# Kernel optimization log

Hardware: AMD Instinct MI355X
Metric: run time of the kernel (lower is better)

## Reference

```python
import jax, jax.numpy as jnp
import numpy as np

NORM = 20.0   # from dataset 'NETS'
ALPHA = 1.0
EPS = 1e-12   # torch F.normalize eps


def _l2_normalize(x):
    n = jnp.sqrt(jnp.sum(x * x, axis=-1, keepdims=True))
    return x / jnp.maximum(n, EPS)


def setup_inputs() -> dict:
    key = jax.random.key(0)
    k1, k2, k3, k4, k5 = jax.random.split(key, 5)
    B, P, C = 4096, 32, 512
    predicted_score = jax.random.uniform(k1, (B,), dtype=jnp.float32) * NORM
    targets = jax.random.uniform(k2, (B,), dtype=jnp.float32) * NORM
    feats = jax.random.normal(k3, (B, C), dtype=jnp.float32)
    pivot_features = jax.random.normal(k4, (B, P, C), dtype=jnp.float32)
    pivot_scores = jax.random.uniform(k5, (B, P), dtype=jnp.float32) * NORM
    return {
        "predicted_score": predicted_score,
        "targets": targets,
        "feats": feats,
        "pivot_features": pivot_features,
        "pivot_scores": pivot_scores,
    }


def reference(predicted_score, targets, feats, pivot_features, pivot_scores):
    scale = ALPHA * NORM
    f = _l2_normalize(feats)                      # (B, C)
    pf = _l2_normalize(pivot_features)            # (B, P, C)
    ps = pivot_scores.astype(jnp.float32)         # (B, P)

    # image-text: (B,1,C) @ (B,C,P) -> (B,P)
    it_matches = jnp.einsum('bc,bpc->bp', f, pf)
    it_label = 1.0 - 2.0 * jnp.abs(targets[:, None] - ps) / scale
    image_text_loss = jnp.mean(jnp.abs(it_matches - it_label))

    # image-image: (B,B)
    ii_matches = f @ f.T
    ii_label = 1.0 - 2.0 * jnp.abs(targets[:, None] - targets[None, :]) / scale
    image_image_loss = jnp.mean(jnp.abs(ii_matches - ii_label))

    # text-text: (B,P,P)
    tt_matches = jnp.einsum('bpc,bqc->bpq', pf, pf)
    tt_label = 1.0 - 2.0 * jnp.abs(ps[:, :, None] - ps[:, None, :]) / scale
    text_text_loss = jnp.mean(jnp.abs(tt_matches - tt_label))

    mae_loss = jnp.mean(jnp.abs(predicted_score - targets))

    return (image_image_loss, text_text_loss, image_text_loss, mae_loss)
```

## Files before the change

kernel.cpp:

```cpp
#include <hip/hip_runtime.h>
#include <hip/hip_bf16.h>
#include <stdint.h>

#define B_N 4096
#define P_N 32
#define C_N 512
#define LABC 0.1f

typedef float  floatx4 __attribute__((ext_vector_type(4)));
typedef __bf16 bf16x8  __attribute__((ext_vector_type(8)));

__device__ __forceinline__ unsigned short f2bf(float x) {
    return __builtin_bit_cast(unsigned short, __float2bfloat16(x));
}
__device__ __forceinline__ float bf2f(unsigned short b) {
    return __builtin_bit_cast(float, ((unsigned int)b) << 16);
}

__device__ __forceinline__ void bfly_reduce2(float& a, float& b) {
#pragma unroll
    for (int m = 1; m < 64; m <<= 1) {
        a += __shfl_xor(a, m, 64);
        b += __shfl_xor(b, m, 64);
    }
}
__device__ __forceinline__ void bfly_reduce1(float& a) {
#pragma unroll
    for (int m = 1; m < 64; m <<= 1) a += __shfl_xor(a, m, 64);
}

__global__ void k_init(double* acc) {
    if (threadIdx.x < 3) acc[threadIdx.x] = 0.0;
}

__global__ __launch_bounds__(256) void k_norm_feats(const float* __restrict__ feats,
                                                    unsigned short* __restrict__ fb) {
    const int wave = threadIdx.x >> 6, lane = threadIdx.x & 63;
    const int row = blockIdx.x * 4 + wave;
    const float* src = feats + (size_t)row * C_N + lane * 8;
    float4 v0 = *(const float4*)src;
    float4 v1 = *(const float4*)(src + 4);
    float ss = v0.x*v0.x + v0.y*v0.y + v0.z*v0.z + v0.w*v0.w
             + v1.x*v1.x + v1.y*v1.y + v1.z*v1.z + v1.w*v1.w;
    bfly_reduce1(ss);
    const float inv = rsqrtf(fmaxf(ss, 1e-24f));
    unsigned short o[8];
    o[0] = f2bf(v0.x*inv); o[1] = f2bf(v0.y*inv); o[2] = f2bf(v0.z*inv); o[3] = f2bf(v0.w*inv);
    o[4] = f2bf(v1.x*inv); o[5] = f2bf(v1.y*inv); o[6] = f2bf(v1.z*inv); o[7] = f2bf(v1.w*inv);
    uint4 pk;
    pk.x = (unsigned)o[0] | ((unsigned)o[1] << 16);
    pk.y = (unsigned)o[2] | ((unsigned)o[3] << 16);
    pk.z = (unsigned)o[4] | ((unsigned)o[5] << 16);
    pk.w = (unsigned)o[6] | ((unsigned)o[7] << 16);
    *(uint4*)(fb + (size_t)row * C_N + lane * 8) = pk;
}

#define CH_STRIDE 33
__global__ __launch_bounds__(256) void k_tt_it(const float* __restrict__ pf_g,
                                               const float* __restrict__ ps_g,
                                               const float* __restrict__ targets,
                                               const unsigned short* __restrict__ fb,
                                               double* __restrict__ acc) {
    __shared__ __align__(16) unsigned short pfs[64 * CH_STRIDE * 8];
    __shared__ float psS[P_N];
    __shared__ float redT[4], redI[4];

    const int b = blockIdx.x;
    const int tid = threadIdx.x, wave = tid >> 6, lane = tid & 63;
    const int quad = lane >> 4, l15 = lane & 15;

    if (tid < P_N) psS[tid] = ps_g[b * P_N + tid];
    const float tb = targets[b];

    uint4 fraw = *(const uint4*)(fb + (size_t)b * C_N + lane * 8);
    const unsigned short* fbits = (const unsigned short*)&fraw;
    float fr[8];
#pragma unroll
    for (int j = 0; j < 8; ++j) fr[j] = bf2f(fbits[j]);

    float it_sum = 0.f;
    const float* base = pf_g + (size_t)b * P_N * C_N;

#pragma unroll
    for (int i = 0; i < 8; ++i) {
        const int r = wave * 8 + i;
        const float* src = base + r * C_N + lane * 8;
        float4 v0 = *(const float4*)src;
        float4 v1 = *(const float4*)(src + 4);
        float pv[8] = {v0.x, v0.y, v0.z, v0.w, v1.x, v1.y, v1.z, v1.w};
        float ss = 0.f, fd = 0.f;
#pragma unroll
        for (int j = 0; j < 8; ++j) { ss += pv[j]*pv[j]; fd += pv[j]*fr[j]; }
        bfly_reduce2(ss, fd);
        const float inv = rsqrtf(fmaxf(ss, 1e-24f));
        unsigned short o[8];
#pragma unroll
        for (int j = 0; j < 8; ++j) o[j] = f2bf(pv[j] * inv);
        uint4 pk;
        pk.x = (unsigned)o[0] | ((unsigned)o[1] << 16);
        pk.y = (unsigned)o[2] | ((unsigned)o[3] << 16);
        pk.z = (unsigned)o[4] | ((unsigned)o[5] << 16);
        pk.w = (unsigned)o[6] | ((unsigned)o[7] << 16);
        *(uint4*)&pfs[((size_t)lane * CH_STRIDE + r) * 8] = pk;
        if (lane == 0) {
            const float lab = 1.f - LABC * fabsf(tb - ps_g[b * P_N + r]);
            it_sum += fabsf(fd * inv - lab);
        }
    }
    __syncthreads();

    const int pt = (wave >> 1) * 16, qt = (wave & 1) * 16;
    floatx4 acc4 = {0.f, 0.f, 0.f, 0.f};
#pragma unroll
    for (int kk = 0; kk < 16; ++kk) {
        const int ch = kk * 4 + quad;
        bf16x8 a = __builtin_bit_cast(bf16x8, *(const uint4*)&pfs[((size_t)ch * CH_STRIDE + pt + l15) * 8]);
        bf16x8 bb = __builtin_bit_cast(bf16x8, *(const uint4*)&pfs[((size_t)ch * CH_STRIDE + qt + l15) * 8]);
        acc4 = __builtin_amdgcn_mfma_f32_16x16x32_bf16(a, bb, acc4, 0, 0, 0);
    }
    float tt_sum = 0.f;
#pragma unroll
    for (int r = 0; r < 4; ++r) {
        const int p = pt + quad * 4 + r;
        const int q = qt + l15;
        const float lab = 1.f - LABC * fabsf(psS[p] - psS[q]);
        tt_sum += fabsf(acc4[r] - lab);
    }

    bfly_reduce2(tt_sum, it_sum);
    if (lane == 0) { redT[wave] = tt_sum; redI[wave] = it_sum; }
    __syncthreads();
    if (tid == 0) {
        atomicAdd(&acc[1], (double)(redT[0] + redT[1] + redT[2] + redT[3]));
        atomicAdd(&acc[2], (double)(redI[0] + redI[1] + redI[2] + redI[3]));
    }
}

#define APAD 130
__global__ __launch_bounds__(256) void k_ii(const unsigned short* __restrict__ fb,
                                            const float* __restrict__ targets,
                                            double* __restrict__ acc) {
    const int bm = blockIdx.y, bn = blockIdx.x;
    if (bn < bm) return;
    __shared__ __align__(16) unsigned short As[4 * APAD * 8];
    __shared__ __align__(16) unsigned short Bs[4 * APAD * 8];
    __shared__ float tmS[128], tnS[128];
    __shared__ float red[4];

    const int tid = threadIdx.x, wave = tid >> 6, lane = tid & 63;
    const int quad = lane >> 4, l15 = lane & 15;
    const int wr = wave >> 1, wc = wave & 1;
    const int mbase = bm * 128, nbase = bn * 128;

    if (tid < 128) tmS[tid] = targets[mbase + tid];
    else           tnS[tid - 128] = targets[nbase + tid - 128];

    const int row = tid >> 1, half = tid & 1;
    const unsigned short* aSrc = fb + (size_t)(mbase + row) * C_N + half * 16;
    const unsigned short* bSrc = fb + (size_t)(nbase + row) * C_N + half * 16;
    const int c0 = half * 2, c1 = half * 2 + 1;

    floatx4 accv[16];
#pragma unroll
    for (int i = 0; i < 16; ++i) accv[i] = (floatx4){0.f, 0.f, 0.f, 0.f};

    uint4 a0 = *(const uint4*)(aSrc);
    uint4 a1 = *(const uint4*)(aSrc + 8);
    uint4 b0 = *(const uint4*)(bSrc);
    uint4 b1 = *(const uint4*)(bSrc + 8);

    for (int ks = 0; ks < 16; ++ks) {
        __syncthreads();
        *(uint4*)&As[((size_t)c0 * APAD + row) * 8] = a0;
        *(uint4*)&As[((size_t)c1 * APAD + row) * 8] = a1;
        *(uint4*)&Bs[((size_t)c0 * APAD + row) * 8] = b0;
        *(uint4*)&Bs[((size_t)c1 * APAD + row) * 8] = b1;
        __syncthreads();
        if (ks < 15) {
            const int off = (ks + 1) * 32;
            a0 = *(const uint4*)(aSrc + off);
            a1 = *(const uint4*)(aSrc + off + 8);
            b0 = *(const uint4*)(bSrc + off);
            b1 = *(const uint4*)(bSrc + off + 8);
        }
        bf16x8 af[4], bfv[4];
#pragma unroll
        for (int t = 0; t < 4; ++t)
            af[t] = __builtin_bit_cast(bf16x8, *(const uint4*)&As[((size_t)quad * APAD + wr * 64 + t * 16 + l15) * 8]);
#pragma unroll
        for (int t = 0; t < 4; ++t)
            bfv[t] = __builtin_bit_cast(bf16x8, *(const uint4*)&Bs[((size_t)quad * APAD + wc * 64 + t * 16 + l15) * 8]);
#pragma unroll
        for (int ti = 0; ti < 4; ++ti)
#pragma unroll
            for (int tj = 0; tj < 4; ++tj)
                accv[ti * 4 + tj] = __builtin_amdgcn_mfma_f32_16x16x32_bf16(af[ti], bfv[tj], accv[ti * 4 + tj], 0, 0, 0);
    }

    float s = 0.f;
#pragma unroll
    for (int ti = 0; ti < 4; ++ti) {
#pragma unroll
        for (int tj = 0; tj < 4; ++tj) {
#pragma unroll
            for (int r = 0; r < 4; ++r) {
                const int p = wr * 64 + ti * 16 + quad * 4 + r;
                const int q = wc * 64 + tj * 16 + l15;
                const float lab = 1.f - LABC * fabsf(tmS[p] - tnS[q]);
                s += fabsf(accv[ti * 4 + tj][r] - lab);
            }
        }
    }
    if (bm != bn) s *= 2.f;
    bfly_reduce1(s);
    if (lane == 0) red[wave] = s;
    __syncthreads();
    if (tid == 0) atomicAdd(&acc[0], (double)(red[0] + red[1] + red[2] + red[3]));
}

__global__ __launch_bounds__(256) void k_final(const float* __restrict__ pred,
                                               const float* __restrict__ targ,
                                               const double* __restrict__ acc,
                                               float* __restrict__ out) {
    __shared__ float red[4];
    const int tid = threadIdx.x, wave = tid >> 6, lane = tid & 63;
    float s = 0.f;
    for (int i = tid; i < B_N; i += 256) s += fabsf(pred[i] - targ[i]);
    bfly_reduce1(s);
    if (lane == 0) red[wave] = s;
    __syncthreads();
    if (tid == 0) {
        const float mae = (red[0] + red[1] + red[2] + red[3]) * (1.f / B_N);
        out[0] = (float)(acc[0] / (double)((size_t)B_N * B_N));
        out[1] = (float)(acc[1] / (double)((size_t)B_N * P_N * P_N));
        out[2] = (float)(acc[2] / (double)((size_t)B_N * P_N));
        out[3] = mae;
    }
}

extern "C" void kernel_launch(void* const* d_in, const int* in_sizes, int n_in,
                              void* d_out, int out_size, void* d_ws, size_t ws_size,
                              hipStream_t stream) {
    const float* pred  = (const float*)d_in[0];
    const float* targ  = (const float*)d_in[1];
    const float* feats = (const float*)d_in[2];
    const float* pf    = (const float*)d_in[3];
    const float* ps    = (const float*)d_in[4];
    float* out = (float*)d_out;

    double* acc = (double*)d_ws;
    unsigned short* fb = (unsigned short*)((char*)d_ws + 256);

    k_init<<<1, 64, 0, stream>>>(acc);
    k_norm_feats<<<B_N / 4, 256, 0, stream>>>(feats, fb);
    k_tt_it<<<B_N, 256, 0, stream>>>(pf, ps, targ, fb, acc);
    k_ii<<<dim3(32, 32), 256, 0, stream>>>(fb, targ, acc);
    k_final<<<1, 256, 0, stream>>>(pred, targ, acc, out);
}
```

Baseline: 448.6 us.

## Fuse ii and tt/it kernels into one launch, normalize pivots via Gram diagonal

Merges the image-image GEMM blocks (upper triangle only, 528 blocks) and the per-sample text-text/image-text blocks into a single kernel sharing a union of shared memory. Pivot features are packed to bf16 unnormalized, and norms come from the Gram matrix diagonal. The image-text dot products are computed with an extra MFMA instead of butterfly reductions. Init and MAE partial sums fold into the prep kernel, cutting launches from five to three and removing per-row shuffle reductions. The risk is extra bf16 rounding because pivots are normalized after the bf16 matmul.

```diff
diff --git a/kernel.cpp b/kernel.cpp
--- a/kernel.cpp
+++ b/kernel.cpp
@@ -6,6 +6,7 @@
 #define P_N 32
 #define C_N 512
 #define LABC 0.1f
+#define N_II 528
 
 typedef float  floatx4 __attribute__((ext_vector_type(4)));
 typedef __bf16 bf16x8  __attribute__((ext_vector_type(8)));
@@ -13,10 +14,14 @@
 __device__ __forceinline__ unsigned short f2bf(float x) {
     return __builtin_bit_cast(unsigned short, __float2bfloat16(x));
 }
-__device__ __forceinline__ float bf2f(unsigned short b) {
-    return __builtin_bit_cast(float, ((unsigned int)b) << 16);
-}
-
+__device__ __forceinline__ uint4 pack8(const float4& v0, const float4& v1) {
+    uint4 pk;
+    pk.x = (unsigned)f2bf(v0.x) | ((unsigned)f2bf(v0.y) << 16);
+    pk.y = (unsigned)f2bf(v0.z) | ((unsigned)f2bf(v0.w) << 16);
+    pk.z = (unsigned)f2bf(v1.x) | ((unsigned)f2bf(v1.y) << 16);
+    pk.w = (unsigned)f2bf(v1.z) | ((unsigned)f2bf(v1.w) << 16);
+    return pk;
+}
 __device__ __forceinline__ void bfly_reduce2(float& a, float& b) {
 #pragma unroll
     for (int m = 1; m < 64; m <<= 1) {
@@ -29,12 +34,12 @@
     for (int m = 1; m < 64; m <<= 1) a += __shfl_xor(a, m, 64);
 }
 
-__global__ void k_init(double* acc) {
-    if (threadIdx.x < 3) acc[threadIdx.x] = 0.0;
-}
-
-__global__ __launch_bounds__(256) void k_norm_feats(const float* __restrict__ feats,
-                                                    unsigned short* __restrict__ fb) {
+__global__ __launch_bounds__(256) void k_prep(const float* __restrict__ feats,
+                                              const float* __restrict__ pred,
+                                              const float* __restrict__ targ,
+                                              unsigned short* __restrict__ fb,
+                                              double* __restrict__ acc,
+                                              float* __restrict__ maePart) {
     const int wave = threadIdx.x >> 6, lane = threadIdx.x & 63;
     const int row = blockIdx.x * 4 + wave;
     const float* src = feats + (size_t)row * C_N + lane * 8;
@@ -44,197 +49,200 @@
              + v1.x*v1.x + v1.y*v1.y + v1.z*v1.z + v1.w*v1.w;
     bfly_reduce1(ss);
     const float inv = rsqrtf(fmaxf(ss, 1e-24f));
-    unsigned short o[8];
-    o[0] = f2bf(v0.x*inv); o[1] = f2bf(v0.y*inv); o[2] = f2bf(v0.z*inv); o[3] = f2bf(v0.w*inv);
-    o[4] = f2bf(v1.x*inv); o[5] = f2bf(v1.y*inv); o[6] = f2bf(v1.z*inv); o[7] = f2bf(v1.w*inv);
-    uint4 pk;
-    pk.x = (unsigned)o[0] | ((unsigned)o[1] << 16);
-    pk.y = (unsigned)o[2] | ((unsigned)o[3] << 16);
-    pk.z = (unsigned)o[4] | ((unsigned)o[5] << 16);
-    pk.w = (unsigned)o[6] | ((unsigned)o[7] << 16);
-    *(uint4*)(fb + (size_t)row * C_N + lane * 8) = pk;
-}
-
-#define CH_STRIDE 33
-__global__ __launch_bounds__(256) void k_tt_it(const float* __restrict__ pf_g,
+    float4 n0 = {v0.x*inv, v0.y*inv, v0.z*inv, v0.w*inv};
+    float4 n1 = {v1.x*inv, v1.y*inv, v1.z*inv, v1.w*inv};
+    *(uint4*)(fb + (size_t)row * C_N + lane * 8) = pack8(n0, n1);
+
+    if (wave == 0) {
+        float v = 0.f;
+        if (lane < 4) {
+            const int r = blockIdx.x * 4 + lane;
+            v = fabsf(pred[r] - targ[r]);
+        }
+        v += __shfl_xor(v, 1, 64);
+        v += __shfl_xor(v, 2, 64);
+        if (lane == 0) maePart[blockIdx.x] = v;
+    }
+    if (blockIdx.x == 0 && threadIdx.x < 3) acc[threadIdx.x] = 0.0;
+}
+
+#define APAD 130
+struct TTsm {
+    unsigned short pfs[64 * 33 * 8];
+    float psS[P_N];
+    float rdiag[P_N];
+    float redT[4], redI[4];
+};
+struct IIsm {
+    unsigned short As[4 * APAD * 8];
+    unsigned short Bs[4 * APAD * 8];
+    float tm[128], tn[128];
+    float red[4];
+};
+union SMu { TTsm tt; IIsm ii; };
+
+__global__ __launch_bounds__(256) void k_fused(const float* __restrict__ pf_g,
                                                const float* __restrict__ ps_g,
                                                const float* __restrict__ targets,
                                                const unsigned short* __restrict__ fb,
                                                double* __restrict__ acc) {
-    __shared__ __align__(16) unsigned short pfs[64 * CH_STRIDE * 8];
-    __shared__ float psS[P_N];
-    __shared__ float redT[4], redI[4];
-
-    const int b = blockIdx.x;
+    __shared__ __align__(16) SMu sm;
     const int tid = threadIdx.x, wave = tid >> 6, lane = tid & 63;
     const int quad = lane >> 4, l15 = lane & 15;
 
-    if (tid < P_N) psS[tid] = ps_g[b * P_N + tid];
-    const float tb = targets[b];
-
-    uint4 fraw = *(const uint4*)(fb + (size_t)b * C_N + lane * 8);
-    const unsigned short* fbits = (const unsigned short*)&fraw;
-    float fr[8];
-#pragma unroll
-    for (int j = 0; j < 8; ++j) fr[j] = bf2f(fbits[j]);
-
-    float it_sum = 0.f;
-    const float* base = pf_g + (size_t)b * P_N * C_N;
-
-#pragma unroll
-    for (int i = 0; i < 8; ++i) {
-        const int r = wave * 8 + i;
-        const float* src = base + r * C_N + lane * 8;
-        float4 v0 = *(const float4*)src;
-        float4 v1 = *(const float4*)(src + 4);
-        float pv[8] = {v0.x, v0.y, v0.z, v0.w, v1.x, v1.y, v1.z, v1.w};
-        float ss = 0.f, fd = 0.f;
-#pragma unroll
-        for (int j = 0; j < 8; ++j) { ss += pv[j]*pv[j]; fd += pv[j]*fr[j]; }
-        bfly_reduce2(ss, fd);
-        const float inv = rsqrtf(fmaxf(ss, 1e-24f));
-        unsigned short o[8];
-#pragma unroll
-        for (int j = 0; j < 8; ++j) o[j] = f2bf(pv[j] * inv);
-        uint4 pk;
-        pk.x = (unsigned)o[0] | ((unsigned)o[1] << 16);
-        pk.y = (unsigned)o[2] | ((unsigned)o[3] << 16);
-        pk.z = (unsigned)o[4] | ((unsigned)o[5] << 16);
-        pk.w = (unsigned)o[6] | ((unsigned)o[7] << 16);
-        *(uint4*)&pfs[((size_t)lane * CH_STRIDE + r) * 8] = pk;
-        if (lane == 0) {
-            const float lab = 1.f - LABC * fabsf(tb - ps_g[b * P_N + r]);
-            it_sum += fabsf(fd * inv - lab);
-        }
-    }
-    __syncthreads();
-
-    const int pt = (wave >> 1) * 16, qt = (wave & 1) * 16;
-    floatx4 acc4 = {0.f, 0.f, 0.f, 0.f};
-#pragma unroll
-    for (int kk = 0; kk < 16; ++kk) {
-        const int ch = kk * 4 + quad;
-        bf16x8 a = __builtin_bit_cast(bf16x8, *(const uint4*)&pfs[((size_t)ch * CH_STRIDE + pt + l15) * 8]);
-        bf16x8 bb = __builtin_bit_cast(bf16x8, *(const uint4*)&pfs[((size_t)ch * CH_STRIDE + qt + l15) * 8]);
-        acc4 = __builtin_amdgcn_mfma_f32_16x16x32_bf16(a, bb, acc4, 0, 0, 0);
-    }
-    float tt_sum = 0.f;
-#pragma unroll
-    for (int r = 0; r < 4; ++r) {
-        const int p = pt + quad * 4 + r;
-        const int q = qt + l15;
-        const float lab = 1.f - LABC * fabsf(psS[p] - psS[q]);
-        tt_sum += fabsf(acc4[r] - lab);
-    }
-
-    bfly_reduce2(tt_sum, it_sum);
-    if (lane == 0) { redT[wave] = tt_sum; redI[wave] = it_sum; }
-    __syncthreads();
-    if (tid == 0) {
-        atomicAdd(&acc[1], (double)(redT[0] + redT[1] + redT[2] + redT[3]));
-        atomicAdd(&acc[2], (double)(redI[0] + redI[1] + redI[2] + redI[3]));
-    }
-}
-
-#define APAD 130
-__global__ __launch_bounds__(256) void k_ii(const unsigned short* __restrict__ fb,
-                                            const float* __restrict__ targets,
-                                            double* __restrict__ acc) {
-    const int bm = blockIdx.y, bn = blockIdx.x;
-    if (bn < bm) return;
-    __shared__ __align__(16) unsigned short As[4 * APAD * 8];
-    __shared__ __align__(16) unsigned short Bs[4 * APAD * 8];
-    __shared__ float tmS[128], tnS[128];
-    __shared__ float red[4];
-
-    const int tid = threadIdx.x, wave = tid >> 6, lane = tid & 63;
-    const int quad = lane >> 4, l15 = lane & 15;
-    const int wr = wave >> 1, wc = wave & 1;
-    const int mbase = bm * 128, nbase = bn * 128;
-
-    if (tid < 128) tmS[tid] = targets[mbase + tid];
-    else           tnS[tid - 128] = targets[nbase + tid - 128];
-
-    const int row = tid >> 1, half = tid & 1;
-    const unsigned short* aSrc = fb + (size_t)(mbase + row) * C_N + half * 16;
-    const unsigned short* bSrc = fb + (size_t)(nbase + row) * C_N + half * 16;
-    const int c0 = half * 2, c1 = half * 2 + 1;
-
-    floatx4 accv[16];
-#pragma unroll
-    for (int i = 0; i < 16; ++i) accv[i] = (floatx4){0.f, 0.f, 0.f, 0.f};
-
-    uint4 a0 = *(const uint4*)(aSrc);
-    uint4 a1 = *(const uint4*)(aSrc + 8);
-    uint4 b0 = *(const uint4*)(bSrc);
-    uint4 b1 = *(const uint4*)(bSrc + 8);
-
-    for (int ks = 0; ks < 16; ++ks) {
-        __syncthreads();
-        *(uint4*)&As[((size_t)c0 * APAD + row) * 8] = a0;
-        *(uint4*)&As[((size_t)c1 * APAD + row) * 8] = a1;
-        *(uint4*)&Bs[((size_t)c0 * APAD + row) * 8] = b0;
-        *(uint4*)&Bs[((size_t)c1 * APAD + row) * 8] = b1;
-        __syncthreads();
-        if (ks < 15) {
-            const int off = (ks + 1) * 32;
-            a0 = *(const uint4*)(aSrc + off);
-            a1 = *(const uint4*)(aSrc + off + 8);
-            b0 = *(const uint4*)(bSrc + off);
-            b1 = *(const uint4*)(bSrc + off + 8);
-        }
-        bf16x8 af[4], bfv[4];
-#pragma unroll
-        for (int t = 0; t < 4; ++t)
-            af[t] = __builtin_bit_cast(bf16x8, *(const uint4*)&As[((size_t)quad * APAD + wr * 64 + t * 16 + l15) * 8]);
-#pragma unroll
-        for (int t = 0; t < 4; ++t)
-            bfv[t] = __builtin_bit_cast(bf16x8, *(const uint4*)&Bs[((size_t)quad * APAD + wc * 64 + t * 16 + l15) * 8]);
+    if (blockIdx.x < N_II) {
+        IIsm& S = sm.ii;
+        int bm = 0, rem = blockIdx.x;
+        while (rem >= 32 - bm) { rem -= 32 - bm; ++bm; }
+        const int bn = bm + rem;
+        const int wr = wave >> 1, wc = wave & 1;
+        const int mbase = bm * 128, nbase = bn * 128;
+
+        if (tid < 128) S.tm[tid] = targets[mbase + tid];
+        else           S.tn[tid - 128] = targets[nbase + tid - 128];
+
+        const int row = tid >> 1, half = tid & 1;
+        const unsigned short* aSrc = fb + (size_t)(mbase + row) * C_N + half * 16;
+        const unsigned short* bSrc = fb + (size_t)(nbase + row) * C_N + half * 16;
+        const int c0 = half * 2, c1 = half * 2 + 1;
+
+        floatx4 accv[16];
+#pragma unroll
+        for (int i = 0; i < 16; ++i) accv[i] = (floatx4){0.f, 0.f, 0.f, 0.f};
+
+        uint4 a0 = *(const uint4*)(aSrc);
+        uint4 a1 = *(const uint4*)(aSrc + 8);
+        uint4 b0 = *(const uint4*)(bSrc);
+        uint4 b1 = *(const uint4*)(bSrc + 8);
+
+        for (int ks = 0; ks < 16; ++ks) {
+            __syncthreads();
+            *(uint4*)&S.As[((size_t)c0 * APAD + row) * 8] = a0;
+            *(uint4*)&S.As[((size_t)c1 * APAD + row) * 8] = a1;
+            *(uint4*)&S.Bs[((size_t)c0 * APAD + row) * 8] = b0;
+            *(uint4*)&S.Bs[((size_t)c1 * APAD + row) * 8] = b1;
+            __syncthreads();
+            if (ks < 15) {
+                const int off = (ks + 1) * 32;
+                a0 = *(const uint4*)(aSrc + off);
+                a1 = *(const uint4*)(aSrc + off + 8);
+                b0 = *(const uint4*)(bSrc + off);
+                b1 = *(const uint4*)(bSrc + off + 8);
+            }
+            bf16x8 af[4], bfv[4];
+#pragma unroll
+            for (int t = 0; t < 4; ++t)
+                af[t] = __builtin_bit_cast(bf16x8, *(const uint4*)&S.As[((size_t)quad * APAD + wr * 64 + t * 16 + l15) * 8]);
+#pragma unroll
+            for (int t = 0; t < 4; ++t)
+                bfv[t] = __builtin_bit_cast(bf16x8, *(const uint4*)&S.Bs[((size_t)quad * APAD + wc * 64 + t * 16 + l15) * 8]);
+#pragma unroll
+            for (int ti = 0; ti < 4; ++ti)
+#pragma unroll
+                for (int tj = 0; tj < 4; ++tj)
+                    accv[ti * 4 + tj] = __builtin_amdgcn_mfma_f32_16x16x32_bf16(af[ti], bfv[tj], accv[ti * 4 + tj], 0, 0, 0);
+        }
+
+        float s = 0.f;
 #pragma unroll
         for (int ti = 0; ti < 4; ++ti)
 #pragma unroll
             for (int tj = 0; tj < 4; ++tj)
-                accv[ti * 4 + tj] = __builtin_amdgcn_mfma_f32_16x16x32_bf16(af[ti], bfv[tj], accv[ti * 4 + tj], 0, 0, 0);
-    }
-
-    float s = 0.f;
-#pragma unroll
-    for (int ti = 0; ti < 4; ++ti) {
-#pragma unroll
-        for (int tj = 0; tj < 4; ++tj) {
-#pragma unroll
-            for (int r = 0; r < 4; ++r) {
-                const int p = wr * 64 + ti * 16 + quad * 4 + r;
-                const int q = wc * 64 + tj * 16 + l15;
-                const float lab = 1.f - LABC * fabsf(tmS[p] - tnS[q]);
-                s += fabsf(accv[ti * 4 + tj][r] - lab);
+#pragma unroll
+                for (int r = 0; r < 4; ++r) {
+                    const int p = wr * 64 + ti * 16 + quad * 4 + r;
+                    const int q = wc * 64 + tj * 16 + l15;
+                    const float lab = 1.f - LABC * fabsf(S.tm[p] - S.tn[q]);
+                    s += fabsf(accv[ti * 4 + tj][r] - lab);
+                }
+        if (bm != bn) s *= 2.f;
+        bfly_reduce1(s);
+        if (lane == 0) S.red[wave] = s;
+        __syncthreads();
+        if (tid == 0) atomicAdd(&acc[0], (double)(S.red[0] + S.red[1] + S.red[2] + S.red[3]));
+    } else {
+        TTsm& S = sm.tt;
+        const int b = blockIdx.x - N_II;
+
+        if (tid < P_N) S.psS[tid] = ps_g[b * P_N + tid];
+        const float tb = targets[b];
+
+        const float* base = pf_g + (size_t)b * P_N * C_N;
+#pragma unroll
+        for (int i = 0; i < 8; ++i) {
+            const int r = wave * 8 + i;
+            const float* src = base + r * C_N + lane * 8;
+            float4 v0 = *(const float4*)src;
+            float4 v1 = *(const float4*)(src + 4);
+            *(uint4*)&S.pfs[((size_t)lane * 33 + r) * 8] = pack8(v0, v1);
+        }
+        if (wave == 0) {
+            uint4 f = *(const uint4*)(fb + (size_t)b * C_N + lane * 8);
+            *(uint4*)&S.pfs[((size_t)lane * 33 + 32) * 8] = f;
+        }
+        __syncthreads();
+
+        const int pt = (wave >> 1) * 16, qt = (wave & 1) * 16;
+        const bool doF = (wave < 2);
+        floatx4 acc4 = {0.f, 0.f, 0.f, 0.f};
+        floatx4 accF = {0.f, 0.f, 0.f, 0.f};
+        const uint4 zero4 = {0u, 0u, 0u, 0u};
+#pragma unroll
+        for (int kk = 0; kk < 16; ++kk) {
+            const int ch = kk * 4 + quad;
+            bf16x8 a = __builtin_bit_cast(bf16x8, *(const uint4*)&S.pfs[((size_t)ch * 33 + pt + l15) * 8]);
+            bf16x8 bb = __builtin_bit_cast(bf16x8, *(const uint4*)&S.pfs[((size_t)ch * 33 + qt + l15) * 8]);
+            acc4 = __builtin_amdgcn_mfma_f32_16x16x32_bf16(a, bb, acc4, 0, 0, 0);
+            if (doF) {
+                uint4 fr = *(const uint4*)&S.pfs[((size_t)ch * 33 + 32) * 8];
+                bf16x8 af = __builtin_bit_cast(bf16x8, (l15 == 0) ? fr : zero4);
+                accF = __builtin_amdgcn_mfma_f32_16x16x32_bf16(af, bb, accF, 0, 0, 0);
             }
         }
-    }
-    if (bm != bn) s *= 2.f;
-    bfly_reduce1(s);
-    if (lane == 0) red[wave] = s;
-    __syncthreads();
-    if (tid == 0) atomicAdd(&acc[0], (double)(red[0] + red[1] + red[2] + red[3]));
-}
-
-__global__ __launch_bounds__(256) void k_final(const float* __restrict__ pred,
-                                               const float* __restrict__ targ,
-                                               const double* __restrict__ acc,
+        if (pt == qt) {
+            if ((l15 >> 2) == quad) S.rdiag[pt + l15] = rsqrtf(fmaxf(acc4[l15 & 3], 1e-24f));
+        }
+        __syncthreads();
+
+        float tt_sum = 0.f, it_sum = 0.f;
+#pragma unroll
+        for (int r = 0; r < 4; ++r) {
+            const int p = pt + quad * 4 + r;
+            const int q = qt + l15;
+            const float val = acc4[r] * S.rdiag[p] * S.rdiag[q];
+            const float lab = 1.f - LABC * fabsf(S.psS[p] - S.psS[q]);
+            tt_sum += fabsf(val - lab);
+        }
+        if (doF && quad == 0) {
+            const int q = qt + l15;
+            const float val = accF[0] * S.rdiag[q];
+            const float lab = 1.f - LABC * fabsf(tb - S.psS[q]);
+            it_sum = fabsf(val - lab);
+        }
+        bfly_reduce2(tt_sum, it_sum);
+        if (lane == 0) { S.redT[wave] = tt_sum; S.redI[wave] = it_sum; }
+        __syncthreads();
+        if (tid == 0) {
+            atomicAdd(&acc[1], (double)(S.redT[0] + S.redT[1] + S.redT[2] + S.redT[3]));
+            atomicAdd(&acc[2], (double)(S.redI[0] + S.redI[1] + S.redI[2] + S.redI[3]));
+        }
+    }
+}
+
+__global__ __launch_bounds__(256) void k_final(const double* __restrict__ acc,
+                                               const float* __restrict__ maePart,
                                                float* __restrict__ out) {
     __shared__ float red[4];
     const int tid = threadIdx.x, wave = tid >> 6, lane = tid & 63;
-    float s = 0.f;
-    for (int i = tid; i < B_N; i += 256) s += fabsf(pred[i] - targ[i]);
+    float s = maePart[tid] + maePart[tid + 256] + maePart[tid + 512] + maePart[tid + 768];
     bfly_reduce1(s);
     if (lane == 0) red[wave] = s;
     __syncthreads();
     if (tid == 0) {
-        const float mae = (red[0] + red[1] + red[2] + red[3]) * (1.f / B_N);
         out[0] = (float)(acc[0] / (double)((size_t)B_N * B_N));
         out[1] = (float)(acc[1] / (double)((size_t)B_N * P_N * P_N));
         out[2] = (float)(acc[2] / (double)((size_t)B_N * P_N));
-        out[3] = mae;
+        out[3] = (red[0] + red[1] + red[2] + red[3]) * (1.f / B_N);
     }
 }
 
@@ -248,12 +256,11 @@
     const float* ps    = (const float*)d_in[4];
     float* out = (float*)d_out;
 
-    double* acc = (double*)d_ws;
-    unsigned short* fb = (unsigned short*)((char*)d_ws + 256);
-
-    k_init<<<1, 64, 0, stream>>>(acc);
-    k_norm_feats<<<B_N / 4, 256, 0, stream>>>(feats, fb);
-    k_tt_it<<<B_N, 256, 0, stream>>>(pf, ps, targ, fb, acc);
-    k_ii<<<dim3(32, 32), 256, 0, stream>>>(fb, targ, acc);
-    k_final<<<1, 256, 0, stream>>>(pred, targ, acc, out);
-}
+    double* acc         = (double*)d_ws;
+    float* maePart      = (float*)((char*)d_ws + 256);
+    unsigned short* fb  = (unsigned short*)((char*)d_ws + 8192);
+
+    k_prep<<<B_N / 4, 256, 0, stream>>>(feats, pred, targ, fb, acc, maePart);
+    k_fused<<<N_II + B_N, 256, 0, stream>>>(pf, ps, targ, fb, acc);
+    k_final<<<1, 256, 0, stream>>>(acc, maePart, out);
+}
```

Result: faster. 412.8 us (-8.0%).
